# Optimization experiments

Hardware: AMD Instinct MI355X
Metric: run time of the kernel (lower is better)

Reference implementation:

```python
import jax, jax.numpy as jnp
import numpy as np
from jax import lax

T_DATA = 4096
SUB = 1024
T_HIST = 64
HIST_BASIS = 4
FIX_VAR = 1.0


def setup_inputs() -> dict:
    key = jax.random.key(0)
    ks = jax.random.split(key, 6)
    return {
        "S_conv": jax.random.normal(ks[0], (T_DATA, SUB), dtype=jnp.float32) * 0.5,
        "up_mu_Z": jax.random.normal(ks[1], (T_DATA, SUB), dtype=jnp.float32) * 0.5,
        "noise": jax.random.normal(ks[2], (T_DATA, SUB), dtype=jnp.float32),
        "W_sub": jnp.ones((SUB,), jnp.float32) * 0.25,
        "theta_syn": jax.random.normal(ks[3], (SUB,), dtype=jnp.float32) * 0.1,
        "theta_spike": jnp.ones((SUB,), jnp.float32) * (-1.0),
        "W_spike": jnp.ones((SUB,), jnp.float32) * 1.0,
        "tau_hist": jnp.arange(0.5, 0.5 + HIST_BASIS * 0.5, 0.5, dtype=jnp.float32),
        "K_hist": jax.random.normal(ks[4], (SUB, HIST_BASIS), dtype=jnp.float32) * 0.1,
        "delta_hist": jax.random.uniform(ks[5], (SUB,), dtype=jnp.float32) * 3.0,
    }


def _hist_kernel(tau_hist, K_hist, delta_hist):
    # alpha-function basis kernels: (t/tau) * exp(-t/tau), shifted by delta, clipped at 0
    t = jnp.arange(T_HIST, dtype=jnp.float32)                     # [T_hist]
    tt = jnp.maximum(t[None, :] - delta_hist[:, None], 0.0)      # [sub, T_hist]
    tau = jnp.exp(tau_hist)                                       # [basis]
    ttau = tt[:, :, None] / tau[None, None, :]                    # [sub, T_hist, basis]
    kern = jnp.sum(ttau * jnp.exp(-ttau) * K_hist[:, None, :], axis=-1)  # [sub, T_hist]
    return kern


def _forward(S_conv, up_mu_Z, noise, W_sub, theta_syn, theta_spike, W_spike,
             tau_hist, K_hist, delta_hist):
    kern = _hist_kernel(tau_hist, K_hist, delta_hist)  # kern[s, lag], lag 0 = most recent spike
    # torch flips the kernel then uses conv1d (cross-correlation) over an
    # oldest-first history buffer; equivalent to dotting oldest-first history
    # with the reversed kernel.
    kern_rev = kern[:, ::-1]                           # [sub, T_hist]
    sigma = FIX_VAR ** 0.5

    def step(hist, xs):
        # hist: [sub, T_hist] spike history, oldest first (index T_hist-1 = newest)
        s_t, up_t, n_t = xs
        filtered = jnp.einsum("st,st->s", hist, kern_rev)
        X_in = s_t + filtered + theta_syn
        X_out = jax.nn.sigmoid(X_in)
        Y_t = X_out * W_sub
        down_t = X_out * W_spike + theta_spike
        # (up*prec + down*prec) / (2*prec) == (up + down) / 2
        mu_t = 0.5 * (up_t + down_t)
        Z_out = jax.nn.sigmoid(mu_t + n_t * sigma)
        hist = jnp.concatenate([hist[:, 1:], Z_out[:, None]], axis=1)
        return hist, (Y_t, Z_out, mu_t, down_t)

    hist0 = jnp.zeros((SUB, T_HIST), S_conv.dtype)
    _, (Y, Z, mu_Z, down_mu_Z) = lax.scan(step, hist0, (S_conv, up_mu_Z, noise))
    return Y, Z, mu_Z, down_mu_Z


def reference(S_conv, up_mu_Z, noise, W_sub, theta_syn, theta_spike, W_spike,
              tau_hist, K_hist, delta_hist):
    return _forward(S_conv, up_mu_Z, noise, W_sub, theta_syn, theta_spike,
                    W_spike, tau_hist, K_hist, delta_hist)
```

## Files before the change

kernel.cpp:

```cpp
#include <hip/hip_runtime.h>

#define NL2E (-1.4426950408889634f)

__device__ __forceinline__ float rl(float v, int lane) {
    return __int_as_float(__builtin_amdgcn_readlane(__float_as_int(v), lane));
}

__global__ __launch_bounds__(64) void leaf_integ_kernel(
    const float* __restrict__ S_conv, const float* __restrict__ up_mu_Z,
    const float* __restrict__ noise, const float* __restrict__ W_sub,
    const float* __restrict__ theta_syn, const float* __restrict__ theta_spike,
    const float* __restrict__ W_spike, const float* __restrict__ tau_hist,
    const float* __restrict__ K_hist, const float* __restrict__ delta_hist,
    float* __restrict__ out)
{
    const int SUB = 1024;
    int bid = blockIdx.x;
    int s = ((bid & 7) << 7) + (bid >> 3);
    int l = threadIdx.x;

    __shared__ float lds_rev[128];

    float thsyn = theta_syn[s];
    float thspk = theta_spike[s];
    float wsub  = W_sub[s];
    float wspk  = W_spike[s];
    float delta = delta_hist[s];

    float tt = fmaxf((float)l - delta, 0.0f);
    float kern = 0.0f;
    #pragma unroll
    for (int b = 0; b < 4; ++b) {
        float rtau = __expf(-tau_hist[b]);
        float ttau = tt * rtau;
        kern += ttau * __expf(-ttau) * K_hist[s * 4 + b];
    }
    float kvs = NL2E * kern;
    lds_rev[63 - l]  = kvs;
    lds_rev[127 - l] = kvs;
    __syncthreads();

    const float* krow = &lds_rev[64 - l];

    float thsynS = NL2E * thsyn;
    float c1 = NL2E * 0.5f * wspk;

    float s0raw = S_conv[(size_t)l * SUB + s];
    float s1raw = S_conv[(size_t)(64 + l) * SUB + s];
    float up0   = up_mu_Z[(size_t)l * SUB + s];
    float n0    = noise[(size_t)l * SUB + s];

    float A    = fmaf(s0raw, NL2E, thsynS);
    float sA   = fmaf(s1raw, NL2E, thsynS);
    float preA = NL2E * (fmaf(0.5f, up0, 0.5f * thspk) + n0);
    float upA  = up0;

    float ab = rl(A, 0);
    float pb = rl(preA, 0);

    float xcap = 0.0f, zcap = 0.0f;

    float* Yo = out;
    float* Zo = out + 4194304;
    float* Mo = out + 8388608;
    float* Do = out + 12582912;

    for (int m = 0; m < 64; ++m) {
        int t0 = m * 64;
        int tP = min(t0 + 128 + l, 4095);
        int tQ = min(t0 + 64 + l, 4095);
        float sB  = S_conv[(size_t)tP * SUB + s];
        float upB = up_mu_Z[(size_t)tQ * SUB + s];
        float nB  = noise[(size_t)tQ * SUB + s];

        #pragma unroll
        for (int j = 0; j < 64; ++j) {
            float ab_nx = rl(A, (j + 1) & 63);
            float pb_nx = (j < 63) ? rl(preA, j + 1) : pb;

            float e1 = __builtin_amdgcn_exp2f(ab);
            float kv = krow[j];
            float xo = __builtin_amdgcn_rcpf(1.0f + e1);
            float vv = fmaf(xo, c1, pb);
            float e2 = __builtin_amdgcn_exp2f(vv);
            float z  = __builtin_amdgcn_rcpf(1.0f + e2);

            bool sel = (l == j);
            xcap = sel ? xo : xcap;
            zcap = sel ? z  : zcap;
            float base = sel ? sA : A;
            A = fmaf(kv, z, base);

            ab = ab_nx;
            pb = pb_nx;
        }

        float down = fmaf(xcap, wspk, thspk);
        float Yv   = xcap * wsub;
        float mu   = 0.5f * (upA + down);
        size_t o = (size_t)(t0 + l) * SUB + s;
        Yo[o] = Yv; Zo[o] = zcap; Mo[o] = mu; Do[o] = down;

        sA   = fmaf(sB, NL2E, thsynS);
        preA = NL2E * (fmaf(0.5f, upB, 0.5f * thspk) + nB);
        upA  = upB;
        pb   = rl(preA, 0);
    }
}

extern "C" void kernel_launch(void* const* d_in, const int* in_sizes, int n_in,
                              void* d_out, int out_size, void* d_ws, size_t ws_size,
                              hipStream_t stream) {
    const float* S_conv     = (const float*)d_in[0];
    const float* up_mu_Z    = (const float*)d_in[1];
    const float* noise      = (const float*)d_in[2];
    const float* W_sub      = (const float*)d_in[3];
    const float* theta_syn  = (const float*)d_in[4];
    const float* theta_spike= (const float*)d_in[5];
    const float* W_spike    = (const float*)d_in[6];
    const float* tau_hist   = (const float*)d_in[7];
    const float* K_hist     = (const float*)d_in[8];
    const float* delta_hist = (const float*)d_in[9];
    float* out = (float*)d_out;

    leaf_integ_kernel<<<dim3(1024), dim3(64), 0, stream>>>(
        S_conv, up_mu_Z, noise, W_sub, theta_syn, theta_spike, W_spike,
        tau_hist, K_hist, delta_hist, out);
}
```

Before: 144.2 us.

## Process two timesteps per iteration by splitting the serial recurrence across wave halves

Restructures the per-timestep serial recurrence so each inner iteration advances two timesteps. The low and high half-waves compute the even and odd step sigmoids in parallel, with a forward correction using the first kernel taps. This shortens the dependent exp/rcp chain per step and halves the inner loop trip count. In exchange it adds extra FMAs and readlanes, a per-block LDS write of the pre-activations, and bpermute calls to gather the captured outputs. It also makes the ordering and correctness logic more intricate.

```diff
diff --git a/kernel.cpp b/kernel.cpp
--- a/kernel.cpp
+++ b/kernel.cpp
@@ -4,6 +4,9 @@
 
 __device__ __forceinline__ float rl(float v, int lane) {
     return __int_as_float(__builtin_amdgcn_readlane(__float_as_int(v), lane));
+}
+__device__ __forceinline__ float bperm(int byteaddr, float v) {
+    return __int_as_float(__builtin_amdgcn_ds_bpermute(byteaddr, __float_as_int(v)));
 }
 
 __global__ __launch_bounds__(64) void leaf_integ_kernel(
@@ -18,8 +21,14 @@
     int bid = blockIdx.x;
     int s = ((bid & 7) << 7) + (bid >> 3);
     int l = threadIdx.x;
+    bool hi = (l >= 32);
+    int pidx = hi ? 1 : 0;
+    int rimR = l >> 1;
+    int rimC = l & 31;
+    int bpaddr = ((((l & 1) ? 32 : 0) + (l >> 1)) << 2);
 
     __shared__ float lds_rev[128];
+    __shared__ float preLds[64];
 
     float thsyn = theta_syn[s];
     float thspk = theta_spike[s];
@@ -40,6 +49,12 @@
     lds_rev[127 - l] = kvs;
     __syncthreads();
 
+    float k0v = rl(kvs, 0);
+    float k1v = rl(kvs, 1);
+    float k2v = rl(kvs, 2);
+    float kca = hi ? k2v : k1v;
+    float kcb = hi ? k1v : k0v;
+
     const float* krow = &lds_rev[64 - l];
 
     float thsynS = NL2E * thsyn;
@@ -55,18 +70,23 @@
     float preA = NL2E * (fmaf(0.5f, up0, 0.5f * thspk) + n0);
     float upA  = up0;
 
-    float ab = rl(A, 0);
-    float pb = rl(preA, 0);
-
-    float xcap = 0.0f, zcap = 0.0f;
+    float ab01 = hi ? rl(A, 1) : rl(A, 0);
+    float xoP  = __builtin_amdgcn_rcpf(1.0f + __builtin_amdgcn_exp2f(ab01));
+    float abN  = hi ? rl(A, 3) : rl(A, 2);
 
     float* Yo = out;
     float* Zo = out + 4194304;
     float* Mo = out + 8388608;
     float* Do = out + 12582912;
 
-    for (int m = 0; m < 64; ++m) {
-        int t0 = m * 64;
+    float xcapH = 0.0f, zcapH = 0.0f;
+    float pbP = 0.0f;
+
+    for (int B = 0; B < 64; ++B) {
+        int t0 = B * 64;
+        preLds[l] = preA;
+        pbP = hi ? rl(preA, 1) : rl(preA, 0);
+
         int tP = min(t0 + 128 + l, 4095);
         int tQ = min(t0 + 64 + l, 4095);
         float sB  = S_conv[(size_t)tP * SUB + s];
@@ -74,26 +94,41 @@
         float nB  = noise[(size_t)tQ * SUB + s];
 
         #pragma unroll
-        for (int j = 0; j < 64; ++j) {
-            float ab_nx = rl(A, (j + 1) & 63);
-            float pb_nx = (j < 63) ? rl(preA, j + 1) : pb;
+        for (int i = 0; i < 32; ++i) {
+            float klo = krow[2 * i];
+            float khi = krow[2 * i + 1];
+            float pbN = (i < 31) ? preLds[2 * i + 2 + pidx] : 0.0f;
 
-            float e1 = __builtin_amdgcn_exp2f(ab);
-            float kv = krow[j];
-            float xo = __builtin_amdgcn_rcpf(1.0f + e1);
-            float vv = fmaf(xo, c1, pb);
+            float vv = fmaf(xoP, c1, pbP);
             float e2 = __builtin_amdgcn_exp2f(vv);
-            float z  = __builtin_amdgcn_rcpf(1.0f + e2);
+            float zP = __builtin_amdgcn_rcpf(1.0f + e2);
 
-            bool sel = (l == j);
-            xcap = sel ? xo : xcap;
-            zcap = sel ? z  : zcap;
-            float base = sel ? sA : A;
-            A = fmaf(kv, z, base);
+            bool cap = (rimC == i);
+            xcapH = cap ? xoP : xcapH;
+            zcapH = cap ? zP  : zcapH;
 
-            ab = ab_nx;
-            pb = pb_nx;
+            float z0 = rl(zP, 0);
+            float z1 = rl(zP, 32);
+
+            float Ab = (rimR == i) ? sA : A;
+            Ab = fmaf(klo, z0, Ab);
+            A  = fmaf(khi, z1, Ab);
+
+            abN = fmaf(kca, z0, abN);
+            abN = fmaf(kcb, z1, abN);
+
+            float e1 = __builtin_amdgcn_exp2f(abN);
+            xoP = __builtin_amdgcn_rcpf(1.0f + e1);
+
+            float alo = rl(A, (2 * i + 4) & 63);
+            float ahi = rl(A, (2 * i + 5) & 63);
+            abN = hi ? ahi : alo;
+
+            pbP = pbN;
         }
+
+        float xcap = bperm(bpaddr, xcapH);
+        float zcap = bperm(bpaddr, zcapH);
 
         float down = fmaf(xcap, wspk, thspk);
         float Yv   = xcap * wsub;
@@ -104,7 +139,6 @@
         sA   = fmaf(sB, NL2E, thsynS);
         preA = NL2E * (fmaf(0.5f, upB, 0.5f * thspk) + nB);
         upA  = upB;
-        pb   = rl(preA, 0);
     }
 }
 
```

Result: faster. 130.4 us (-9.6%).
